# Kernel tuning notes

Hardware: AMD Instinct MI355X
Metric: run time of the kernel (lower is better)

Reference implementation:

```python
import jax, jax.numpy as jnp
import numpy as np

EPS = 1e-5

def layernorm(x, g, b):
    mu = jnp.mean(x, axis=-1, keepdims=True)
    var = jnp.mean(jnp.square(x - mu), axis=-1, keepdims=True)
    return (x - mu) * jax.lax.rsqrt(var + EPS) * g + b

def rope(x):
    # x: [B, H, S, hd]; faithful to source: theta = 10000**(-2*pos/hd), pos in {0,2,4,...}
    S, hd = x.shape[-2], x.shape[-1]
    pos2 = jnp.arange(0, hd, 2, dtype=jnp.float32)
    theta = jnp.power(10000.0, -2.0 * pos2 / hd)          # [hd/2]
    ang = jnp.arange(S, dtype=jnp.float32)[:, None] * theta  # [S, hd/2]
    cos, sin = jnp.cos(ang), jnp.sin(ang)                  # broadcast over B,H
    xr = x.reshape(*x.shape[:-1], hd // 2, 2)
    x0, x1 = xr[..., 0], xr[..., 1]
    out = jnp.stack([x0 * cos - x1 * sin, x1 * cos + x0 * sin], axis=-1)
    return out.reshape(x.shape)

def setup_inputs() -> dict:
    key = jax.random.key(0)
    ks = jax.random.split(key, 8)
    B, S, D, H = 2, 2048, 1024, 16
    hd = D // H
    s_in = 1.0 / np.sqrt(D)
    s_h = 1.0 / np.sqrt(2 * D)
    return {
        "x": jax.random.normal(ks[0], (B, S, D), jnp.float32),
        "ln1_g": jnp.ones((D,), jnp.float32),
        "ln1_b": jnp.zeros((D,), jnp.float32),
        "Wq": jax.random.normal(ks[1], (H, D, hd), jnp.float32) * s_in,
        "Wk": jax.random.normal(ks[2], (H, D, hd), jnp.float32) * s_in,
        "Wv": jax.random.normal(ks[3], (H, D, hd), jnp.float32) * s_in,
        "Wo": jax.random.normal(ks[4], (D, D), jnp.float32) * s_in,
        "ln2_g": jnp.ones((D,), jnp.float32),
        "ln2_b": jnp.zeros((D,), jnp.float32),
        "W1": jax.random.normal(ks[5], (D, 2 * D), jnp.float32) * s_in,
        "W2": jax.random.normal(ks[6], (D, 2 * D), jnp.float32) * s_in,
        "W3": jax.random.normal(ks[7], (2 * D, D), jnp.float32) * s_h,
    }

def reference(x, ln1_g, ln1_b, Wq, Wk, Wv, Wo, ln2_g, ln2_b, W1, W2, W3):
    B, S, D = x.shape
    # --- attention sublayer ---
    h = layernorm(x, ln1_g, ln1_b)
    q = jnp.einsum("bsd,hdk->bhsk", h, Wq)
    k = jnp.einsum("bsd,hdk->bhsk", h, Wk)
    v = jnp.einsum("bsd,hdk->bhsk", h, Wv)
    q, k = rope(q), rope(k)
    hd = q.shape[-1]
    scores = jnp.einsum("bhqk,bhsk->bhqs", q, k) * (hd ** -0.5)  # [B,H,S,S]
    causal = jnp.tril(jnp.ones((S, S), bool))
    scores = jnp.where(causal, scores, jnp.float32(-jnp.inf))
    attn = jax.nn.softmax(scores, axis=-1)
    o = jnp.einsum("bhqs,bhsk->bhqk", attn, v)                   # [B,H,S,hd]
    o = o.transpose(0, 2, 1, 3).reshape(B, S, D)                 # concat heads
    x = x + o @ Wo
    # --- SwiGLU FFN sublayer ---
    h2 = layernorm(x, ln2_g, ln2_b)
    u = h2 @ W1
    ffn = (u * jax.nn.sigmoid(u)) * (h2 @ W2)
    return x + ffn @ W3
```

## Files before the change

kernel.cpp:

```cpp
#include <hip/hip_runtime.h>
#include <hip/hip_bf16.h>

using bf16 = __hip_bfloat16;
typedef __attribute__((ext_vector_type(8))) short bf16x8;
typedef __attribute__((ext_vector_type(4))) float f32x4;


__device__ inline float toF(float x) { return x; }
__device__ inline float toF(bf16 x) { return __bfloat162float(x); }

__device__ __forceinline__ void unpack8(uint4 u, float* f) {
    f[0] = __uint_as_float(u.x << 16); f[1] = __uint_as_float(u.x & 0xffff0000u);
    f[2] = __uint_as_float(u.y << 16); f[3] = __uint_as_float(u.y & 0xffff0000u);
    f[4] = __uint_as_float(u.z << 16); f[5] = __uint_as_float(u.z & 0xffff0000u);
    f[6] = __uint_as_float(u.w << 16); f[7] = __uint_as_float(u.w & 0xffff0000u);
}

__device__ __forceinline__ uint4 packbf8(const float* f) {
    union { unsigned short u[8]; uint4 v; } r;
#pragma unroll
    for (int i = 0; i < 8; i++) {
        bf16 b = __float2bfloat16(f[i]);
        r.u[i] = *(unsigned short*)&b;
    }
    return r.v;
}

__device__ __forceinline__ unsigned pack2(float lo, float hi) {
    bf16 a = __float2bfloat16(lo), b = __float2bfloat16(hi);
    return ((unsigned)*(unsigned short*)&b << 16) | (unsigned)*(unsigned short*)&a;
}

__device__ __forceinline__ void gl_lds16(const void* g, void* l) {
    __builtin_amdgcn_global_load_lds(
        (__attribute__((address_space(1))) void*)g,
        (__attribute__((address_space(3))) void*)l, 16, 0, 0);
}

template <typename Tx>
__device__ __forceinline__ void ln_body(
    const Tx* __restrict__ x, const float* __restrict__ g,
    const float* __restrict__ b, bf16* __restrict__ out, int row,
    float* s1, float* s2)
{
    const int D = 1024;
    int tid = threadIdx.x;
    const Tx* xr = x + (size_t)row * D;

    float vals[4];
    float sum = 0.f, sumsq = 0.f;
#pragma unroll
    for (int i = 0; i < 4; i++) {
        float v = toF(xr[tid + i * 256]);
        vals[i] = v; sum += v; sumsq += v * v;
    }
#pragma unroll
    for (int off = 32; off > 0; off >>= 1) {
        sum += __shfl_xor(sum, off);
        sumsq += __shfl_xor(sumsq, off);
    }
    int wave = tid >> 6, lane = tid & 63;
    if (lane == 0) { s1[wave] = sum; s2[wave] = sumsq; }
    __syncthreads();
    sum = s1[0] + s1[1] + s1[2] + s1[3];
    sumsq = s2[0] + s2[1] + s2[2] + s2[3];

    float mu = sum * (1.f / D);
    float var = sumsq * (1.f / D) - mu * mu;
    float rstd = rsqrtf(var + 1e-5f);

    bf16* orow = out + (size_t)row * D;
#pragma unroll
    for (int i = 0; i < 4; i++) {
        int c = tid + i * 256;
        orow[c] = __float2bfloat16((vals[i] - mu) * rstd * g[c] + b[c]);
    }
}

__global__ __launch_bounds__(256) void prep1_kernel(
    const float* __restrict__ x, const float* __restrict__ g,
    const float* __restrict__ b, bf16* __restrict__ h0, bf16* __restrict__ h1,
    const float* __restrict__ Wq, const float* __restrict__ Wk,
    const float* __restrict__ Wv, bf16* __restrict__ wt)
{
    __shared__ float t[32][33];
    __shared__ float s1[4], s2[4];
    int bx = blockIdx.x;
    if (bx < 4096) {
        int bb = bx >> 11, row = bx & 2047;
        ln_body<float>(x + ((size_t)bb << 21), g, b, bb ? h1 : h0, row, s1, s2);
        return;
    }
    int zz = bx - 4096;
    int z = zz >> 6, rem = zz & 63;
    int yy = rem >> 1, xx = rem & 1;
    const float* s = (z < 16) ? Wq : (z < 32) ? Wk : Wv;
    const float* ip = s + (size_t)(z & 15) * 65536;
    bf16* op = wt + ((size_t)z << 16);
    int c0 = xx * 32, r0 = yy * 32;
    int tx = threadIdx.x & 31, ty = threadIdx.x >> 5;
#pragma unroll
    for (int i = 0; i < 4; i++)
        t[ty + 8 * i][tx] = ip[(size_t)(r0 + ty + 8 * i) * 64 + c0 + tx];
    __syncthreads();
#pragma unroll
    for (int i = 0; i < 4; i++)
        op[(size_t)(c0 + ty + 8 * i) * 1024 + r0 + tx] = __float2bfloat16(t[tx][ty + 8 * i]);
}

__global__ __launch_bounds__(256) void prep2_kernel(
    const bf16* __restrict__ x2, const float* __restrict__ g,
    const float* __restrict__ b, bf16* __restrict__ h2,
    const float* __restrict__ W1, const float* __restrict__ W2,
    bf16* __restrict__ wt, const float* __restrict__ W3,
    bf16* __restrict__ w3t)
{
    __shared__ float t[32][33];
    __shared__ float s1[4], s2[4];
    int bx = blockIdx.x;
    if (bx < 2048) {
        ln_body<bf16>(x2, g, b, h2, bx, s1, s2);
        return;
    }
    int tx = threadIdx.x & 31, ty = threadIdx.x >> 5;
    int zz = bx - 2048;
    if (zz < 4096) {
        int xx = zz & 63, yy = (zz >> 6) & 31, z = zz >> 11;
        const float* ip = z ? W2 : W1;
        bf16* op = wt + ((size_t)z << 21);
        int c0 = xx * 32, r0 = yy * 32;
#pragma unroll
        for (int i = 0; i < 4; i++)
            t[ty + 8 * i][tx] = ip[(size_t)(r0 + ty + 8 * i) * 2048 + c0 + tx];
        __syncthreads();
#pragma unroll
        for (int i = 0; i < 4; i++)
            op[(size_t)(c0 + ty + 8 * i) * 1024 + r0 + tx] = __float2bfloat16(t[tx][ty + 8 * i]);
        return;
    }
    int idx = zz - 4096;
    int xx = idx & 31, yy = idx >> 5;
    int c0 = xx * 32, r0 = yy * 32;
#pragma unroll
    for (int i = 0; i < 4; i++)
        t[ty + 8 * i][tx] = W3[(size_t)(r0 + ty + 8 * i) * 1024 + c0 + tx];
    __syncthreads();
#pragma unroll
    for (int i = 0; i < 4; i++)
        w3t[(size_t)(c0 + ty + 8 * i) * 2048 + r0 + tx] = __float2bfloat16(t[tx][ty + 8 * i]);
}

__global__ __launch_bounds__(256) void tconv_kernel(
    const float* __restrict__ in, bf16* __restrict__ out, int R, int C)
{
    __shared__ float t[32][33];
    int c0 = blockIdx.x * 32, r0 = blockIdx.y * 32;
    int tx = threadIdx.x & 31, ty = threadIdx.x >> 5;
#pragma unroll
    for (int i = 0; i < 4; i++)
        t[ty + 8 * i][tx] = in[(size_t)(r0 + ty + 8 * i) * C + c0 + tx];
    __syncthreads();
#pragma unroll
    for (int i = 0; i < 4; i++)
        out[(size_t)(c0 + ty + 8 * i) * R + r0 + tx] = __float2bfloat16(t[tx][ty + 8 * i]);
}

__global__ __launch_bounds__(256) void tconv_wo_kernel(
    const float* __restrict__ Wo, bf16* __restrict__ out)
{
    __shared__ float t[32][33];
    int z = blockIdx.z;
    const float* ip = Wo + (size_t)z * 64;
    bf16* op = out + ((size_t)z << 16);
    int c0 = blockIdx.x * 32, r0 = blockIdx.y * 32;
    int tx = threadIdx.x & 31, ty = threadIdx.x >> 5;
#pragma unroll
    for (int i = 0; i < 4; i++)
        t[ty + 8 * i][tx] = ip[(size_t)(r0 + ty + 8 * i) * 1024 + c0 + tx];
    __syncthreads();
#pragma unroll
    for (int i = 0; i < 4; i++)
        op[(size_t)(c0 + ty + 8 * i) * 1024 + r0 + tx] = __float2bfloat16(t[tx][ty + 8 * i]);
}

template <int MODE>
__global__ __launch_bounds__(256) void mfma_gemm(
    const bf16* __restrict__ A, const bf16* __restrict__ BT0,
    void* __restrict__ Cv, const void* __restrict__ resv,
    const void* __restrict__ p5, void* __restrict__ p6,
    int M, int N, int K)
{
    constexpr int NB = (MODE == 5) ? 3 : 2;
    __shared__ bf16 smem[2][NB][64 * 64];
    int tid = threadIdx.x, lane = tid & 63, w = tid >> 6;
    int wm = w >> 1, wn = w & 1;
    int m0 = blockIdx.y * 64, n0 = blockIdx.x * 64;

    const bf16* Ap = A;
    const bf16* BT = BT0;
    bf16* Cq = nullptr;
    const float* resF = (const float*)resv;
    void* Cdst = Cv;
    if (MODE == 1) {
        int z = blockIdx.z;
        if (z >> 1) Ap = (const bf16*)resv;
        BT = BT0 + ((size_t)(z & 1) << 20);
        Cq = (bf16*)((z >> 1) ? p6 : Cv) + ((size_t)(z & 1) << 21);
    }
    if (MODE == 6) Cq = (bf16*)Cv;
    if (MODE == 2) {
        int z = blockIdx.z;
        if (z) { Ap = (const bf16*)p5; Cdst = p6; }
        resF = (const float*)resv + ((size_t)z << 21);
    }

    int lrow = lane >> 3;
    int lcb  = (lane & 7) ^ lrow;
    const bf16* Ag  = Ap + (size_t)(m0 + w * 8 + lrow) * K + lcb * 8;
    const bf16* Bg0 = BT + (size_t)(n0 + w * 8 + lrow) * K + lcb * 8;
    const bf16* B2g = (MODE == 5)
        ? (const bf16*)resv + (size_t)(n0 + w * 8 + lrow) * K + lcb * 8
        : nullptr;
    unsigned sbase = (unsigned)__builtin_amdgcn_readfirstlane(w * 8 * 128);
    char* smc = (char*)smem;

    f32x4 acc[2][2], acc2[2][2];
#pragma unroll
    for (int i = 0; i < 2; i++)
#pragma unroll
        for (int j = 0; j < 2; j++) {
            acc[i][j] = (f32x4){0.f, 0.f, 0.f, 0.f};
            if (MODE == 5) acc2[i][j] = (f32x4){0.f, 0.f, 0.f, 0.f};
        }

    int cidx = lane & 15, quad = lane >> 4;

    auto STAGE = [&](int buf, int k0) {
        char* p = smc + (size_t)buf * (NB * 8192) + sbase;
        gl_lds16(Ag + k0,                   p);
        gl_lds16(Ag + (size_t)32 * K + k0,  p + 4096);
        gl_lds16(Bg0 + k0,                  p + 8192);
        gl_lds16(Bg0 + (size_t)32 * K + k0, p + 12288);
        if (MODE == 5) {
            gl_lds16(B2g + k0,                  p + 16384);
            gl_lds16(B2g + (size_t)32 * K + k0, p + 20480);
        }
    };

    STAGE(0, 0);
    __syncthreads();
    int cur = 0;
    for (int k0 = 0; k0 < K; k0 += 64) {
        if (k0 + 64 < K) STAGE(cur ^ 1, k0 + 64);
        const bf16* Ab = (const bf16*)(smc + (size_t)cur * (NB * 8192));
        const bf16* Bb = Ab + 4096;
        const bf16* B2b = Ab + 8192;
#pragma unroll
        for (int kk = 0; kk < 2; kk++) {
            int pb = (kk * 4 + quad) ^ (cidx & 7);
            bf16x8 af[2], bfr[2], b2f[2];
#pragma unroll
            for (int i = 0; i < 2; i++)
                af[i] = *(const bf16x8*)&Ab[(wm * 32 + i * 16 + cidx) * 64 + pb * 8];
#pragma unroll
            for (int j = 0; j < 2; j++)
                bfr[j] = *(const bf16x8*)&Bb[(wn * 32 + j * 16 + cidx) * 64 + pb * 8];
            if (MODE == 5) {
#pragma unroll
                for (int j = 0; j < 2; j++)
                    b2f[j] = *(const bf16x8*)&B2b[(wn * 32 + j * 16 + cidx) * 64 + pb * 8];
            }
            __builtin_amdgcn_s_setprio(1);
#pragma unroll
            for (int i = 0; i < 2; i++)
#pragma unroll
                for (int j = 0; j < 2; j++) {
                    acc[i][j] = __builtin_amdgcn_mfma_f32_16x16x32_bf16(af[i], bfr[j], acc[i][j], 0, 0, 0);
                    if (MODE == 5)
                        acc2[i][j] = __builtin_amdgcn_mfma_f32_16x16x32_bf16(af[i], b2f[j], acc2[i][j], 0, 0, 0);
                }
            __builtin_amdgcn_s_setprio(0);
        }
        __syncthreads();
        cur ^= 1;
    }

    int rbase = quad * 4;
#pragma unroll
    for (int i = 0; i < 2; i++) {
#pragma unroll
        for (int j = 0; j < 2; j++) {
            int row0 = m0 + wm * 32 + i * 16 + rbase;
            int col = n0 + wn * 32 + j * 16 + cidx;
            if (MODE == 6) {
                int h_ = col >> 6, d = col & 63;
                uint2 t;
                t.x = pack2(acc[i][j][0], acc[i][j][1]);
                t.y = pack2(acc[i][j][2], acc[i][j][3]);
                *(uint2*)&Cq[(size_t)h_ * 131072 + (size_t)d * 2048 + row0] = t;
                continue;
            }
#pragma unroll
            for (int r = 0; r < 4; r++) {
                int row = row0 + r;
                float v = acc[i][j][r];
                size_t idx = (size_t)row * N + col;
                if (MODE == 1) {
                    int h_ = col >> 6, kk = col & 63;
                    float other = __shfl_xor(v, 1);
                    float p = (float)(kk >> 1);
                    float theta = __expf(p * -0.5756462732485114f);
                    float ang = (float)row * theta;
                    float c, sn; __sincosf(ang, &sn, &c);
                    float outv = (kk & 1) ? (v * c + other * sn) : (v * c - other * sn);
                    Cq[((size_t)h_ * 2048 + row) * 64 + kk] = __float2bfloat16(outv);
                } else if (MODE == 2) {
                    v += resF[idx];
                    ((bf16*)Cdst)[idx] = __float2bfloat16(v);
                } else if (MODE == 5) {
                    float g2 = acc2[i][j][r];
                    float sg = 1.f / (1.f + __expf(-v));
                    ((bf16*)Cv)[idx] = __float2bfloat16(v * sg * g2);
                } else {
                    v += __bfloat162float(((const bf16*)resv)[idx]);
                    ((float*)Cv)[idx] = v;
                }
            }
        }
    }
}

__global__ __launch_bounds__(256) void attn_kernel(
    const bf16* __restrict__ q0, const bf16* __restrict__ k0,
    const bf16* __restrict__ vt0, bf16* __restrict__ o0,
    const bf16* __restrict__ q1, const bf16* __restrict__ k1,
    const bf16* __restrict__ vt1, bf16* __restrict__ o1)
{
    const int S = 2048;
    __shared__ bf16 Ks[64 * 64];
    __shared__ bf16 Vs[64 * 64];
    __shared__ __align__(16) char QPbuf[64 * 72 * 2];

    int zb = blockIdx.z;
    const bf16* q = zb ? q1 : q0;
    const bf16* k = zb ? k1 : k0;
    const bf16* vt = zb ? vt1 : vt0;
    bf16* o = zb ? o1 : o0;

    int h = blockIdx.y;
    int qt = (h & 8) ? (int)blockIdx.x : 31 - (int)blockIdx.x;
    int tid = threadIdx.x, lane = tid & 63, w = tid >> 6;
    int quad = lane >> 4, cidx = lane & 15;
    int m0 = qt * 64;

    const bf16* qb = q + ((size_t)h * S + m0) * 64;
    const bf16* kb = k + (size_t)h * S * 64;
    const bf16* vtb = vt + (size_t)h * 64 * S;

    int srow = tid >> 2;
    int sg = (tid & 3) * 16;

    bf16 (*Qs)[72] = (bf16 (*)[72])QPbuf;
    {
        const uint4* src = (const uint4*)(qb + (size_t)srow * 64 + sg);
        uint4 u0 = src[0], u1 = src[1];
        float f[16]; unpack8(u0, f); unpack8(u1, f + 8);
#pragma unroll
        for (int i = 0; i < 16; i++) f[i] *= 0.125f * 1.44269504f;
        *(uint4*)&Qs[srow][sg] = packbf8(f);
        *(uint4*)&Qs[srow][sg + 8] = packbf8(f + 8);
    }
    bf16x8 bQ0 = *(const bf16x8*)&Qs[w * 16 + cidx][quad * 8];
    bf16x8 bQ1 = *(const bf16x8*)&Qs[w * 16 + cidx][32 + quad * 8];

    unsigned* Pst = (unsigned*)QPbuf + w * 576;

    int cb0 = (tid & 3) * 2;
    int sw0 = ((cb0)     ^ (srow & 7)) * 8;
    int sw1 = ((cb0 + 1) ^ (srow & 7)) * 8;
    int pb0 = ((quad)     ^ (cidx & 7)) * 8;
    int pb1 = ((4 + quad) ^ (cidx & 7)) * 8;

    float m_i = -INFINITY, l_i = 0.f;
    f32x4 Oc[4];
#pragma unroll
    for (int i = 0; i < 4; i++) Oc[i] = (f32x4){0.f, 0.f, 0.f, 0.f};

    uint4 ka0, ka1, va0, va1;
    {
        const uint4* ksrc = (const uint4*)(kb + (size_t)srow * 64 + sg);
        ka0 = ksrc[0]; ka1 = ksrc[1];
        const uint4* vsrc = (const uint4*)(vtb + (size_t)srow * S + sg);
        va0 = vsrc[0]; va1 = vsrc[1];
    }

    for (int kt = 0; kt <= qt; kt++) {
        __syncthreads();
        *(uint4*)&Ks[srow * 64 + sw0] = ka0;
        *(uint4*)&Ks[srow * 64 + sw1] = ka1;
        *(uint4*)&Vs[srow * 64 + sw0] = va0;
        *(uint4*)&Vs[srow * 64 + sw1] = va1;
        __syncthreads();
        if (kt < qt) {
            const uint4* kn = (const uint4*)(kb + (size_t)((kt + 1) * 64 + srow) * 64 + sg);
            ka0 = kn[0]; ka1 = kn[1];
            const uint4* vn = (const uint4*)(vtb + (size_t)srow * S + (kt + 1) * 64 + sg);
            va0 = vn[0]; va1 = vn[1];
        }

        f32x4 sc[4];
#pragma unroll
        for (int i = 0; i < 4; i++) {
            bf16x8 aK0 = *(const bf16x8*)&Ks[(i * 16 + cidx) * 64 + pb0];
            bf16x8 aK1 = *(const bf16x8*)&Ks[(i * 16 + cidx) * 64 + pb1];
            f32x4 z = (f32x4){0.f, 0.f, 0.f, 0.f};
            __builtin_amdgcn_s_setprio(1);
            z = __builtin_amdgcn_mfma_f32_16x16x32_bf16(aK0, bQ0, z, 0, 0, 0);
            z = __builtin_amdgcn_mfma_f32_16x16x32_bf16(aK1, bQ1, z, 0, 0, 0);
            __builtin_amdgcn_s_setprio(0);
            sc[i] = z;
        }

        if (kt == qt) {
#pragma unroll
            for (int i = 0; i < 4; i++)
#pragma unroll
                for (int r = 0; r < 4; r++)
                    if (i * 16 + quad * 4 + r > w * 16 + cidx) sc[i][r] = -INFINITY;
        }

        float l0 = fmaxf(fmaxf(sc[0][0], sc[0][1]), fmaxf(sc[0][2], sc[0][3]));
        float l1 = fmaxf(fmaxf(sc[1][0], sc[1][1]), fmaxf(sc[1][2], sc[1][3]));
        float l2 = fmaxf(fmaxf(sc[2][0], sc[2][1]), fmaxf(sc[2][2], sc[2][3]));
        float l3 = fmaxf(fmaxf(sc[3][0], sc[3][1]), fmaxf(sc[3][2], sc[3][3]));
        float lmax = fmaxf(fmaxf(l0, l1), fmaxf(l2, l3));

        if (!__all(lmax <= m_i + 8.f)) {
            float pmax = fmaxf(lmax, __shfl_xor(lmax, 16));
            pmax = fmaxf(pmax, __shfl_xor(pmax, 32));
            float mnew = fmaxf(m_i, pmax);
            float alpha = __builtin_amdgcn_exp2f(m_i - mnew);
            l_i *= alpha;
#pragma unroll
            for (int i = 0; i < 4; i++) {
                Oc[i][0] *= alpha; Oc[i][1] *= alpha;
                Oc[i][2] *= alpha; Oc[i][3] *= alpha;
            }
            m_i = mnew;
        }

        float rs = 0.f;
#pragma unroll
        for (int i = 0; i < 4; i++)
#pragma unroll
            for (int r = 0; r < 4; r++) {
                sc[i][r] = __builtin_amdgcn_exp2f(sc[i][r] - m_i);
                rs += sc[i][r];
            }
        l_i += rs;

#pragma unroll
        for (int i = 0; i < 4; i++) {
            uint2 t;
            t.x = pack2(sc[i][0], sc[i][1]);
            t.y = pack2(sc[i][2], sc[i][3]);
            *(uint2*)&Pst[cidx * 36 + 8 * i + 2 * quad] = t;
        }
        bf16x8 bP0 = *(const bf16x8*)&Pst[cidx * 36 + 4 * quad];
        bf16x8 bP1 = *(const bf16x8*)&Pst[cidx * 36 + 16 + 4 * quad];

#pragma unroll
        for (int i = 0; i < 4; i++) {
            bf16x8 aV0 = *(const bf16x8*)&Vs[(i * 16 + cidx) * 64 + pb0];
            bf16x8 aV1 = *(const bf16x8*)&Vs[(i * 16 + cidx) * 64 + pb1];
            __builtin_amdgcn_s_setprio(1);
            Oc[i] = __builtin_amdgcn_mfma_f32_16x16x32_bf16(aV0, bP0, Oc[i], 0, 0, 0);
            Oc[i] = __builtin_amdgcn_mfma_f32_16x16x32_bf16(aV1, bP1, Oc[i], 0, 0, 0);
            __builtin_amdgcn_s_setprio(0);
        }
    }

    float lr = l_i;
    lr += __shfl_xor(lr, 16);
    lr += __shfl_xor(lr, 32);
    float inv = 1.f / lr;
#pragma unroll
    for (int i = 0; i < 4; i++) {
        uint2 t;
        t.x = pack2(Oc[i][0] * inv, Oc[i][1] * inv);
        t.y = pack2(Oc[i][2] * inv, Oc[i][3] * inv);
        *(uint2*)&Pst[cidx * 36 + 8 * i + 2 * quad] = t;
    }
    int r2 = lane >> 2, g2 = (lane & 3) * 8;
    uint4 o0v = *(const uint4*)&Pst[r2 * 36 + g2];
    uint4 o1v = *(const uint4*)&Pst[r2 * 36 + g2 + 4];
    bf16* orow = o + (size_t)(m0 + w * 16 + r2) * 1024 + h * 64;
    *(uint4*)(orow + g2 * 2) = o0v;
    *(uint4*)(orow + g2 * 2 + 8) = o1v;
}

extern "C" void kernel_launch(void* const* d_in, const int* in_sizes, int n_in,
                              void* d_out, int out_size, void* d_ws, size_t ws_size,
                              hipStream_t stream)
{
    const int S = 2048;

    const float* x    = (const float*)d_in[0];
    const float* ln1g = (const float*)d_in[1];
    const float* ln1b = (const float*)d_in[2];
    const float* Wq   = (const float*)d_in[3];
    const float* Wk   = (const float*)d_in[4];
    const float* Wv   = (const float*)d_in[5];
    const float* Wo   = (const float*)d_in[6];
    const float* ln2g = (const float*)d_in[7];
    const float* ln2b = (const float*)d_in[8];
    const float* W1   = (const float*)d_in[9];
    const float* W2   = (const float*)d_in[10];
    const float* W3   = (const float*)d_in[11];
    float* out = (float*)d_out;

    const size_t M2 = 1u << 21;
    bf16* r0 = (bf16*)d_ws;
    bf16* r1 = r0 + M2;
    bf16* r2 = r1 + M2;
    bf16* r3 = r2 + M2;
    bf16* pb0 = (bf16*)out;
    bf16* pb1 = pb0 + 2 * M2;
    float* out0 = out;
    float* out1 = out + (1u << 21);

    prep1_kernel<<<7168, 256, 0, stream>>>(x, ln1g, ln1b, r0, r1,
                                           Wq, Wk, Wv, pb0);

    mfma_gemm<1><<<dim3(16, 32, 4), 256, 0, stream>>>(
        r0, pb0, r2, r1, nullptr, pb1, S, 1024, 1024);

    mfma_gemm<6><<<dim3(16, 32, 1), 256, 0, stream>>>(
        r0, pb0 + M2, pb0, nullptr, nullptr, nullptr, S, 1024, 1024);

    mfma_gemm<6><<<dim3(16, 32, 1), 256, 0, stream>>>(
        r1, pb0 + M2, r0, nullptr, nullptr, nullptr, S, 1024, 1024);

    attn_kernel<<<dim3(32, 16, 2), 256, 0, stream>>>(
        r2, r3, pb0, r1, pb1, pb1 + M2, r0, pb0 + M2);

    tconv_wo_kernel<<<dim3(2, 32, 16), 256, 0, stream>>>(Wo, r2);

    mfma_gemm<2><<<dim3(16, 32, 2), 256, 0, stream>>>(
        r1, r2, r3, x, pb0 + M2, r0, S, 1024, 1024);

    prep2_kernel<<<8192, 256, 0, stream>>>(r3, ln2g, ln2b, pb1, W1, W2, pb0,
                                           W3, pb1 + M2);

    mfma_gemm<5><<<dim3(32, 32, 1), 256, 0, stream>>>(
        pb1, pb0, r1, pb0 + M2, nullptr, nullptr, S, 2048, 1024);

    mfma_gemm<4><<<dim3(16, 32, 1), 256, 0, stream>>>(
        r1, pb1 + M2, out0, r3, nullptr, nullptr, S, 1024, 2048);

    prep2_kernel<<<6144, 256, 0, stream>>>(r0, ln2g, ln2b, r3, W1, W2, pb1,
                                           nullptr, nullptr);

    mfma_gemm<5><<<dim3(32, 32, 1), 256, 0, stream>>>(
        r3, pb1, r1, pb1 + M2, nullptr, nullptr, S, 2048, 1024);

    tconv_kernel<<<dim3(32, 64), 256, 0, stream>>>(W3, r3, 2048, 1024);

    mfma_gemm<4><<<dim3(16, 32, 1), 256, 0, stream>>>(
        r1, r3, out1, r0, nullptr, nullptr, S, 1024, 2048);
}
```

Measured before the change: 332.9 us.

## Split SwiGLU GEMM into dedicated 128-row kernel and regroup QKV launches

Moves the fused W1/W2 SwiGLU GEMM out of the templated mfma_gemm into a dedicated kernel with 128x64 tiles. Each warp now computes 4x2 fragments for both weights, which reuses each A fragment across more MFMAs and halves the block count. The QKV projection launches are regrouped: MODE 6 now handles both batches through the z dimension, and MODE 1 is split into two launches, with buffer assignments reshuffled to match. The larger SwiGLU tile raises register and LDS use (32KB per stage) and lowers the number of blocks, which may reduce occupancy.

```diff
diff --git a/kernel.cpp b/kernel.cpp
--- a/kernel.cpp
+++ b/kernel.cpp
@@ -190,8 +190,7 @@
     const void* __restrict__ p5, void* __restrict__ p6,
     int M, int N, int K)
 {
-    constexpr int NB = (MODE == 5) ? 3 : 2;
-    __shared__ bf16 smem[2][NB][64 * 64];
+    __shared__ bf16 smem[2][2][64 * 64];
     int tid = threadIdx.x, lane = tid & 63, w = tid >> 6;
     int wm = w >> 1, wn = w & 1;
     int m0 = blockIdx.y * 64, n0 = blockIdx.x * 64;
@@ -203,11 +202,14 @@
     void* Cdst = Cv;
     if (MODE == 1) {
         int z = blockIdx.z;
-        if (z >> 1) Ap = (const bf16*)resv;
-        BT = BT0 + ((size_t)(z & 1) << 20);
-        Cq = (bf16*)((z >> 1) ? p6 : Cv) + ((size_t)(z & 1) << 21);
-    }
-    if (MODE == 6) Cq = (bf16*)Cv;
+        BT = BT0 + ((size_t)z << 20);
+        Cq = (bf16*)(z ? p6 : Cv);
+    }
+    if (MODE == 6) {
+        int z = blockIdx.z;
+        if (z) { Ap = (const bf16*)p5; Cq = (bf16*)p6; }
+        else Cq = (bf16*)Cv;
+    }
     if (MODE == 2) {
         int z = blockIdx.z;
         if (z) { Ap = (const bf16*)p5; Cdst = p6; }
@@ -218,33 +220,23 @@
     int lcb  = (lane & 7) ^ lrow;
     const bf16* Ag  = Ap + (size_t)(m0 + w * 8 + lrow) * K + lcb * 8;
     const bf16* Bg0 = BT + (size_t)(n0 + w * 8 + lrow) * K + lcb * 8;
-    const bf16* B2g = (MODE == 5)
-        ? (const bf16*)resv + (size_t)(n0 + w * 8 + lrow) * K + lcb * 8
-        : nullptr;
     unsigned sbase = (unsigned)__builtin_amdgcn_readfirstlane(w * 8 * 128);
     char* smc = (char*)smem;
 
-    f32x4 acc[2][2], acc2[2][2];
+    f32x4 acc[2][2];
 #pragma unroll
     for (int i = 0; i < 2; i++)
 #pragma unroll
-        for (int j = 0; j < 2; j++) {
-            acc[i][j] = (f32x4){0.f, 0.f, 0.f, 0.f};
-            if (MODE == 5) acc2[i][j] = (f32x4){0.f, 0.f, 0.f, 0.f};
-        }
+        for (int j = 0; j < 2; j++) acc[i][j] = (f32x4){0.f, 0.f, 0.f, 0.f};
 
     int cidx = lane & 15, quad = lane >> 4;
 
     auto STAGE = [&](int buf, int k0) {
-        char* p = smc + (size_t)buf * (NB * 8192) + sbase;
+        char* p = smc + (size_t)buf * 16384 + sbase;
         gl_lds16(Ag + k0,                   p);
         gl_lds16(Ag + (size_t)32 * K + k0,  p + 4096);
         gl_lds16(Bg0 + k0,                  p + 8192);
         gl_lds16(Bg0 + (size_t)32 * K + k0, p + 12288);
-        if (MODE == 5) {
-            gl_lds16(B2g + k0,                  p + 16384);
-            gl_lds16(B2g + (size_t)32 * K + k0, p + 20480);
-        }
     };
 
     STAGE(0, 0);
@@ -252,33 +244,24 @@
     int cur = 0;
     for (int k0 = 0; k0 < K; k0 += 64) {
         if (k0 + 64 < K) STAGE(cur ^ 1, k0 + 64);
-        const bf16* Ab = (const bf16*)(smc + (size_t)cur * (NB * 8192));
+        const bf16* Ab = (const bf16*)(smc + (size_t)cur * 16384);
         const bf16* Bb = Ab + 4096;
-        const bf16* B2b = Ab + 8192;
 #pragma unroll
         for (int kk = 0; kk < 2; kk++) {
             int pb = (kk * 4 + quad) ^ (cidx & 7);
-            bf16x8 af[2], bfr[2], b2f[2];
+            bf16x8 af[2], bfr[2];
 #pragma unroll
             for (int i = 0; i < 2; i++)
                 af[i] = *(const bf16x8*)&Ab[(wm * 32 + i * 16 + cidx) * 64 + pb * 8];
 #pragma unroll
             for (int j = 0; j < 2; j++)
                 bfr[j] = *(const bf16x8*)&Bb[(wn * 32 + j * 16 + cidx) * 64 + pb * 8];
-            if (MODE == 5) {
+            __builtin_amdgcn_s_setprio(1);
+#pragma unroll
+            for (int i = 0; i < 2; i++)
 #pragma unroll
                 for (int j = 0; j < 2; j++)
-                    b2f[j] = *(const bf16x8*)&B2b[(wn * 32 + j * 16 + cidx) * 64 + pb * 8];
-            }
-            __builtin_amdgcn_s_setprio(1);
-#pragma unroll
-            for (int i = 0; i < 2; i++)
-#pragma unroll
-                for (int j = 0; j < 2; j++) {
                     acc[i][j] = __builtin_amdgcn_mfma_f32_16x16x32_bf16(af[i], bfr[j], acc[i][j], 0, 0, 0);
-                    if (MODE == 5)
-                        acc2[i][j] = __builtin_amdgcn_mfma_f32_16x16x32_bf16(af[i], b2f[j], acc2[i][j], 0, 0, 0);
-                }
             __builtin_amdgcn_s_setprio(0);
         }
         __syncthreads();
@@ -317,14 +300,103 @@
                 } else if (MODE == 2) {
                     v += resF[idx];
                     ((bf16*)Cdst)[idx] = __float2bfloat16(v);
-                } else if (MODE == 5) {
-                    float g2 = acc2[i][j][r];
-                    float sg = 1.f / (1.f + __expf(-v));
-                    ((bf16*)Cv)[idx] = __float2bfloat16(v * sg * g2);
                 } else {
                     v += __bfloat162float(((const bf16*)resv)[idx]);
                     ((float*)Cv)[idx] = v;
                 }
+            }
+        }
+    }
+}
+
+__global__ __launch_bounds__(256) void swiglu_gemm(
+    const bf16* __restrict__ A, const bf16* __restrict__ B1T,
+    const bf16* __restrict__ B2T, bf16* __restrict__ C)
+{
+    const int K = 1024, N = 2048;
+    __shared__ bf16 smem[2][16384];
+    int tid = threadIdx.x, lane = tid & 63, w = tid >> 6;
+    int wm = w >> 1, wn = w & 1;
+    int m0 = blockIdx.y * 128, n0 = blockIdx.x * 64;
+
+    int lrow = lane >> 3;
+    int lcb  = (lane & 7) ^ lrow;
+    const bf16* Ag  = A   + (size_t)(m0 + w * 8 + lrow) * K + lcb * 8;
+    const bf16* B1g = B1T + (size_t)(n0 + w * 8 + lrow) * K + lcb * 8;
+    const bf16* B2g = B2T + (size_t)(n0 + w * 8 + lrow) * K + lcb * 8;
+    unsigned sbase = (unsigned)__builtin_amdgcn_readfirstlane(w * 8 * 128);
+    char* smc = (char*)smem;
+
+    f32x4 acc[4][2], acc2[4][2];
+#pragma unroll
+    for (int i = 0; i < 4; i++)
+#pragma unroll
+        for (int j = 0; j < 2; j++) {
+            acc[i][j] = (f32x4){0.f, 0.f, 0.f, 0.f};
+            acc2[i][j] = (f32x4){0.f, 0.f, 0.f, 0.f};
+        }
+
+    int cidx = lane & 15, quad = lane >> 4;
+
+    auto STAGE = [&](int buf, int k0) {
+        char* p = smc + (size_t)buf * 32768 + sbase;
+#pragma unroll
+        for (int n = 0; n < 4; n++)
+            gl_lds16(Ag + (size_t)(n * 32) * K + k0, p + n * 4096);
+#pragma unroll
+        for (int n = 0; n < 2; n++) {
+            gl_lds16(B1g + (size_t)(n * 32) * K + k0, p + 16384 + n * 4096);
+            gl_lds16(B2g + (size_t)(n * 32) * K + k0, p + 24576 + n * 4096);
+        }
+    };
+
+    STAGE(0, 0);
+    __syncthreads();
+    int cur = 0;
+    for (int k0 = 0; k0 < K; k0 += 64) {
+        if (k0 + 64 < K) STAGE(cur ^ 1, k0 + 64);
+        const bf16* Ab = (const bf16*)(smc + (size_t)cur * 32768);
+        const bf16* Bb = Ab + 8192;
+        const bf16* B2b = Ab + 12288;
+#pragma unroll
+        for (int kk = 0; kk < 2; kk++) {
+            int pb = (kk * 4 + quad) ^ (cidx & 7);
+            bf16x8 af[4], bfr[2], b2f[2];
+#pragma unroll
+            for (int i = 0; i < 4; i++)
+                af[i] = *(const bf16x8*)&Ab[(wm * 64 + i * 16 + cidx) * 64 + pb * 8];
+#pragma unroll
+            for (int j = 0; j < 2; j++) {
+                bfr[j] = *(const bf16x8*)&Bb[(wn * 32 + j * 16 + cidx) * 64 + pb * 8];
+                b2f[j] = *(const bf16x8*)&B2b[(wn * 32 + j * 16 + cidx) * 64 + pb * 8];
+            }
+            __builtin_amdgcn_s_setprio(1);
+#pragma unroll
+            for (int i = 0; i < 4; i++)
+#pragma unroll
+                for (int j = 0; j < 2; j++) {
+                    acc[i][j] = __builtin_amdgcn_mfma_f32_16x16x32_bf16(af[i], bfr[j], acc[i][j], 0, 0, 0);
+                    acc2[i][j] = __builtin_amdgcn_mfma_f32_16x16x32_bf16(af[i], b2f[j], acc2[i][j], 0, 0, 0);
+                }
+            __builtin_amdgcn_s_setprio(0);
+        }
+        __syncthreads();
+        cur ^= 1;
+    }
+
+    int rbase = quad * 4;
+#pragma unroll
+    for (int i = 0; i < 4; i++) {
+#pragma unroll
+        for (int j = 0; j < 2; j++) {
+#pragma unroll
+            for (int r = 0; r < 4; r++) {
+                int row = m0 + wm * 64 + i * 16 + rbase + r;
+                int col = n0 + wn * 32 + j * 16 + cidx;
+                float u = acc[i][j][r];
+                float g2 = acc2[i][j][r];
+                float sg = 1.f / (1.f + __expf(-u));
+                C[(size_t)row * N + col] = __float2bfloat16(u * sg * g2);
             }
         }
     }
@@ -532,28 +604,27 @@
     prep1_kernel<<<7168, 256, 0, stream>>>(x, ln1g, ln1b, r0, r1,
                                            Wq, Wk, Wv, pb0);
 
-    mfma_gemm<1><<<dim3(16, 32, 4), 256, 0, stream>>>(
-        r0, pb0, r2, r1, nullptr, pb1, S, 1024, 1024);
-
-    mfma_gemm<6><<<dim3(16, 32, 1), 256, 0, stream>>>(
-        r0, pb0 + M2, pb0, nullptr, nullptr, nullptr, S, 1024, 1024);
-
-    mfma_gemm<6><<<dim3(16, 32, 1), 256, 0, stream>>>(
-        r1, pb0 + M2, r0, nullptr, nullptr, nullptr, S, 1024, 1024);
+    mfma_gemm<6><<<dim3(16, 32, 2), 256, 0, stream>>>(
+        r0, pb0 + M2, pb1, nullptr, r1, pb1 + M2, S, 1024, 1024);
+
+    mfma_gemm<1><<<dim3(16, 32, 2), 256, 0, stream>>>(
+        r0, pb0, r2, nullptr, nullptr, r3, S, 1024, 1024);
+
+    mfma_gemm<1><<<dim3(16, 32, 2), 256, 0, stream>>>(
+        r1, pb0, r0, nullptr, nullptr, pb0 + M2, S, 1024, 1024);
 
     attn_kernel<<<dim3(32, 16, 2), 256, 0, stream>>>(
-        r2, r3, pb0, r1, pb1, pb1 + M2, r0, pb0 + M2);
+        r2, r3, pb1, r1, r0, pb0 + M2, pb1 + M2, pb0);
 
     tconv_wo_kernel<<<dim3(2, 32, 16), 256, 0, stream>>>(Wo, r2);
 
     mfma_gemm<2><<<dim3(16, 32, 2), 256, 0, stream>>>(
-        r1, r2, r3, x, pb0 + M2, r0, S, 1024, 1024);
+        r1, r2, r3, x, pb0, r0, S, 1024, 1024);
 
     prep2_kernel<<<8192, 256, 0, stream>>>(r3, ln2g, ln2b, pb1, W1, W2, pb0,
                                            W3, pb1 + M2);
 
-    mfma_gemm<5><<<dim3(32, 32, 1), 256, 0, stream>>>(
-        pb1, pb0, r1, pb0 + M2, nullptr, nullptr, S, 2048, 1024);
+    swiglu_gemm<<<dim3(32, 16), 256, 0, stream>>>(pb1, pb0, pb0 + M2, r1);
 
     mfma_gemm<4><<<dim3(16, 32, 1), 256, 0, stream>>>(
         r1, pb1 + M2, out0, r3, nullptr, nullptr, S, 1024, 2048);
@@ -561,8 +632,7 @@
     prep2_kernel<<<6144, 256, 0, stream>>>(r0, ln2g, ln2b, r3, W1, W2, pb1,
                                            nullptr, nullptr);
 
-    mfma_gemm<5><<<dim3(32, 32, 1), 256, 0, stream>>>(
-        r3, pb1, r1, pb1 + M2, nullptr, nullptr, S, 2048, 1024);
+    swiglu_gemm<<<dim3(32, 16), 256, 0, stream>>>(r3, pb1, pb1 + M2, r1);
 
     tconv_kernel<<<dim3(32, 64), 256, 0, stream>>>(W3, r3, 2048, 1024);
 
```

New measurement: 312.2 us. 6.2% less time.
